# Kernel tuning notes

Hardware: AMD Instinct MI355X
Metric: run time of the kernel (lower is better)

Reference implementation:

```python
import jax, jax.numpy as jnp
import numpy as np

MIN_NORM = 1e-15
EPS = 1e-7  # artanh domain clamp for fp32


def _tan_k(u, k):
    sk = jnp.sqrt(-k)
    return jnp.tanh(jnp.clip(sk * u, -15.0, 15.0)) / sk


def _artan_k(u, k):
    sk = jnp.sqrt(-k)
    return jnp.arctanh(jnp.clip(sk * u, -1.0 + EPS, 1.0 - EPS)) / sk


def _norm(x):
    return jnp.maximum(jnp.linalg.norm(x, axis=-1, keepdims=True), MIN_NORM)


def mobius_add(x, y, k):
    x2 = jnp.sum(x * x, axis=-1, keepdims=True)
    y2 = jnp.sum(y * y, axis=-1, keepdims=True)
    xy = jnp.sum(x * y, axis=-1, keepdims=True)
    num = (1.0 - 2.0 * k * xy - k * y2) * x + (1.0 + k * x2) * y
    den = 1.0 - 2.0 * k * xy + k * k * x2 * y2
    return num / jnp.maximum(den, MIN_NORM)


def mobius_matvec(M, x, k):
    # x: [..., d_in], M: [d_out, d_in]
    xn = _norm(x)
    mx = x @ M.T
    mxn = _norm(mx)
    res = _tan_k(mxn / xn * _artan_k(xn, k), k) * (mx / mxn)
    return jnp.where(jnp.all(mx == 0.0, axis=-1, keepdims=True), 0.0, res)


def mobius_pointwise_mul(w, x, k):
    xn = _norm(x)
    wx = w * x
    wxn = _norm(wx)
    res = _tan_k(wxn / xn * _artan_k(xn, k), k) * (wx / wxn)
    return jnp.where(jnp.all(wx == 0.0, axis=-1, keepdims=True), 0.0, res)


def expmap0(u, k):
    un = _norm(u)
    return _tan_k(un, k) * u / un


def logmap0(y, k):
    yn = _norm(y)
    return _artan_k(yn, k) * y / yn


def one_rnn_transform(W, h, U, x, b, k):
    Wh = mobius_matvec(W, h, k)
    Ux = mobius_matvec(U, x, k)
    return mobius_add(mobius_add(Wh, Ux, k), b, k)


def mobius_gru_cell(x, hx, w_ih, w_hh, b, k):
    W_ir, W_ih_, W_iz = jnp.split(w_ih, 3, axis=0)
    W_hr, W_hh_, W_hz = jnp.split(w_hh, 3, axis=0)
    b_r, b_h, b_z = b[0], b[1], b[2]
    z_t = jax.nn.sigmoid(logmap0(one_rnn_transform(W_hz, hx, W_iz, x, b_z, k), k))
    r_t = jax.nn.sigmoid(logmap0(one_rnn_transform(W_hr, hx, W_ir, x, b_r, k), k))
    rh_t = mobius_pointwise_mul(r_t, hx, k)
    h_tilde = one_rnn_transform(W_hh_, rh_t, W_ih_, x, b_h, k)
    delta_h = mobius_add(-hx, h_tilde, k)
    return mobius_add(hx, mobius_pointwise_mul(z_t, delta_h, k), k)


def mobius_gru_layer(x_tbd, h0, w_ih, w_hh, b, k, hyperbolic_input):
    # x_tbd: [T, B, D]; h0: [B, H]
    if not hyperbolic_input:
        x_tbd = expmap0(x_tbd, k)

    def step(hx, xt):
        h = expmap0(hx, k)
        h = mobius_gru_cell(xt, h, w_ih, w_hh, b, k)
        h = logmap0(h, k)
        return h, h

    h_last, outs = jax.lax.scan(step, h0, x_tbd)
    return outs, h_last  # outs: [T, B, H]


def setup_inputs() -> dict:
    key = jax.random.key(0)
    ks = jax.random.split(key, 8)
    B, T, D, H = 64, 1024, 256, 256
    stdv = 1.0 / np.sqrt(H)
    x = 0.02 * jax.random.normal(ks[0], (B, T, D), dtype=jnp.float32)
    k = jnp.float32(-1.0)  # hyperbolic curvature (geoopt sign convention)
    h0 = jnp.zeros((2, B, H), dtype=jnp.float32)
    w_ih0 = jax.random.uniform(ks[1], (3 * H, D), jnp.float32, -stdv, stdv)
    w_hh0 = jax.random.uniform(ks[2], (3 * H, H), jnp.float32, -stdv, stdv)
    b0 = 1e-5 * jax.random.normal(ks[3], (3, H), dtype=jnp.float32)
    w_ih1 = jax.random.uniform(ks[4], (3 * H, H), jnp.float32, -stdv, stdv)
    w_hh1 = jax.random.uniform(ks[5], (3 * H, H), jnp.float32, -stdv, stdv)
    b1 = 1e-5 * jax.random.normal(ks[6], (3, H), dtype=jnp.float32)
    return {"x": x, "k": k, "h0": h0, "w_ih0": w_ih0, "w_hh0": w_hh0, "b0": b0,
            "w_ih1": w_ih1, "w_hh1": w_hh1, "b1": b1}


def reference(x, k, h0, w_ih0, w_hh0, b0, w_ih1, w_hh1, b1):
    # x: [B, T, D]; source unbinds dim 1 as time -> scan over time-major.
    xt = jnp.swapaxes(x, 0, 1)  # [T, B, D]
    out0, hl0 = mobius_gru_layer(xt, h0[0], w_ih0, w_hh0, b0, k, hyperbolic_input=False)
    out1, hl1 = mobius_gru_layer(out0, h0[1], w_ih1, w_hh1, b1, k, hyperbolic_input=True)
    ht = jnp.stack([hl0, hl1])  # [num_layers, B, H]
    return out1, ht
```

## Files before the change

### kernel.cpp

```cpp
#include <hip/hip_runtime.h>
#include <cstdint>
#include <cstddef>

#define MINN 1e-15f
#define EPSA 1e-7f
#define C_L2E 1.44269504088896341f
#define C_LN2 0.69314718055994531f

typedef _Float16 half_t;
typedef _Float16 half2_t __attribute__((ext_vector_type(2)));

#if defined(__has_builtin)
#if __has_builtin(__builtin_amdgcn_update_dpp) && __has_builtin(__builtin_amdgcn_readlane)
#define USE_DPP 1
#endif
#endif

__device__ __forceinline__ float fexp2_(float x) {
#if defined(__has_builtin) && __has_builtin(__builtin_amdgcn_exp2f)
    return __builtin_amdgcn_exp2f(x);
#else
    return exp2f(x);
#endif
}
__device__ __forceinline__ float flog2_(float x) {
#if defined(__has_builtin) && __has_builtin(__builtin_amdgcn_logf)
    return __builtin_amdgcn_logf(x);
#else
    return log2f(x);
#endif
}
__device__ __forceinline__ float frcp_(float x) {
#if defined(__has_builtin) && __has_builtin(__builtin_amdgcn_rcpf)
    return __builtin_amdgcn_rcpf(x);
#else
    return 1.f / x;
#endif
}
__device__ __forceinline__ float tan_k_(float u, float sk, float rsk) {
    float a = fminf(fmaxf(sk * u, -15.f), 15.f);
    float t = fexp2_(a * (2.f * C_L2E));
    return (1.f - 2.f * frcp_(t + 1.f)) * rsk;
}
__device__ __forceinline__ float artan_k_(float u, float sk, float rsk) {
    float a = fminf(fmaxf(sk * u, -1.f + EPSA), 1.f - EPSA);
    return flog2_((1.f + a) * frcp_(1.f - a)) * (0.5f * C_LN2) * rsk;
}
__device__ __forceinline__ float sigm_(float x) {
    return frcp_(1.f + fexp2_(-x * C_L2E));
}
__device__ __forceinline__ float wave_sum(float v) {
#pragma unroll
    for (int off = 32; off; off >>= 1) v += __shfl_xor(v, off, 64);
    return v;
}

#ifdef USE_DPP
template <int CTRL, int RM, int BM>
__device__ __forceinline__ float dppmov_(float x) {
    return __builtin_bit_cast(float,
        __builtin_amdgcn_update_dpp(0, __builtin_bit_cast(int, x), CTRL, RM, BM, false));
}
#endif
__device__ __forceinline__ float wsum63_(float x) {
#ifdef USE_DPP
    x += dppmov_<0x111, 0xf, 0xf>(x);
    x += dppmov_<0x112, 0xf, 0xf>(x);
    x += dppmov_<0x114, 0xf, 0xe>(x);
    x += dppmov_<0x118, 0xf, 0xc>(x);
    x += dppmov_<0x142, 0xa, 0xf>(x);
    x += dppmov_<0x143, 0xc, 0xf>(x);
    return x;
#else
    return wave_sum(x);
#endif
}
__device__ __forceinline__ float gsum8_(float x) {
#ifdef USE_DPP
    x += dppmov_<0x111, 0xf, 0xf>(x);
    x += dppmov_<0x112, 0xf, 0xf>(x);
    x += dppmov_<0x114, 0xf, 0xe>(x);
    return x;
#else
    x += __shfl_xor(x, 1, 64);
    x += __shfl_xor(x, 2, 64);
    x += __shfl_xor(x, 4, 64);
    return x;
#endif
}
__device__ __forceinline__ float rdlane_(float x, int l) {
#ifdef USE_DPP
    return __builtin_bit_cast(float,
        __builtin_amdgcn_readlane(__builtin_bit_cast(int, x), l));
#else
    return __shfl(x, l, 64);
#endif
}
template <int N>
__device__ __forceinline__ void bredX(float* v, float* redbuf, int tid) {
    const int lane = tid & 63, wave = tid >> 6;
#pragma unroll
    for (int n = 0; n < N; ++n) {
        float s = wsum63_(v[n]);
        if (lane == 63) redbuf[n * 8 + wave] = s;
    }
    __syncthreads();
    float part = redbuf[lane & (8 * N - 1)];
    part = gsum8_(part);
#pragma unroll
    for (int n = 0; n < N; ++n) v[n] = rdlane_(part, 8 * n + 7);
}

__device__ __forceinline__ float dot2acc(uint32_t w, uint32_t h, float acc) {
#if defined(__has_builtin) && __has_builtin(__builtin_amdgcn_fdot2)
    return __builtin_amdgcn_fdot2(__builtin_bit_cast(half2_t, w),
                                  __builtin_bit_cast(half2_t, h), acc, false);
#else
    half2_t a = __builtin_bit_cast(half2_t, w);
    half2_t b = __builtin_bit_cast(half2_t, h);
    acc = fmaf((float)a[0], (float)b[0], acc);
    return fmaf((float)a[1], (float)b[1], acc);
#endif
}

__global__ __launch_bounds__(256) void kt_transpose(
    const float* __restrict__ a0, const float* __restrict__ a1,
    float* __restrict__ o0, float* __restrict__ o1) {
    int idx = blockIdx.x * 256 + threadIdx.x;
    int m = idx / 196608, rem = idx % 196608;
    int j = rem >> 8, kk = rem & 255;
    const float* in = (m == 0) ? a0 : a1;
    float* outp     = (m == 0) ? o0 : o1;
    outp[kk * 768 + j] = in[j * 256 + kk];
}

__global__ __launch_bounds__(256) void kt_prep1(
    const float* __restrict__ whh0, const float* __restrict__ whh1,
    uint32_t* __restrict__ p0, uint32_t* __restrict__ p1) {
    int idx = blockIdx.x * 256 + threadIdx.x;
    int l = idx >> 16, e = idx & 65535;
    int r4 = e >> 11, rem = e & 2047;
    int t = rem >> 2, m = r4 * 4 + (rem & 3);
    int lane = t & 63, wave = t >> 6;
    int p = wave * 32 + (lane & 31), ph = lane >> 5;
    int g = m >> 6, mi = m & 63;
    int row = g ? (512 + p) : p;
    int i = ph * 128 + 2 * mi;
    const float* w = l ? whh1 : whh0;
    half2_t hv;
    hv[0] = (half_t)w[row * 256 + i];
    hv[1] = (half_t)w[row * 256 + i + 1];
    (l ? p1 : p0)[e] = __builtin_bit_cast(uint32_t, hv);
}

__global__ __launch_bounds__(256) void kt_prep2(
    const float* __restrict__ whh0, const float* __restrict__ whh1,
    uint32_t* __restrict__ p0, uint32_t* __restrict__ p1) {
    int idx = blockIdx.x * 256 + threadIdx.x;
    int l = idx >> 15, e = idx & 32767;
    int i2 = e >> 8, j = e & 255;
    const float* w = l ? whh1 : whh0;
    half2_t hv;
    hv[0] = (half_t)w[(256 + j) * 256 + 2 * i2];
    hv[1] = (half_t)w[(256 + j) * 256 + 2 * i2 + 1];
    (l ? p1 : p0)[e] = __builtin_bit_cast(uint32_t, hv);
}

__global__ __launch_bounds__(256) void kt_init(
    const float* __restrict__ h0, float* __restrict__ hcar) {
    int i = blockIdx.x * 256 + threadIdx.x;
    hcar[i] = h0[i];
}
__global__ __launch_bounds__(256) void kt_final(
    const float* __restrict__ hcar, float* __restrict__ dst) {
    int i = blockIdx.x * 256 + threadIdx.x;
    dst[i] = hcar[i];
}

__global__ __launch_bounds__(256) void kt_rowscale(
    const float* __restrict__ src, long long strideB,
    float* __restrict__ s_arr, float* __restrict__ ax_arr,
    const float* __restrict__ kptr, int mode) {
    int lane = threadIdx.x & 63;
    int r = blockIdx.x * 4 + (threadIdx.x >> 6);
    float k = kptr[0], sk = sqrtf(-k), rsk = frcp_(sk);
    size_t off = (size_t)(r >> 6) * strideB + (size_t)(r & 63) * 256 + lane * 4;
    float4 v = *(const float4*)&src[off];
    float n2 = wave_sum(v.x * v.x + v.y * v.y + v.z * v.z + v.w * v.w);
    float n = sqrtf(n2);
    float s, xn;
    if (mode == 0) {
        float nrm = fmaxf(n, MINN);
        float tk = tan_k_(nrm, sk, rsk);
        s = tk * frcp_(nrm);
        xn = fmaxf(tk * (n * frcp_(nrm)), MINN);
    } else {
        s = 1.f;
        xn = fmaxf(n, MINN);
    }
    float ax = artan_k_(xn, sk, rsk) * frcp_(xn);
    if (lane == 0) { s_arr[r] = s; ax_arr[r] = ax; }
}

__global__ __launch_bounds__(256) void kt_gemm(
    const float* __restrict__ A, long long strideB,
    const float* __restrict__ s_arr,
    const float* __restrict__ Bt, float* __restrict__ C) {
    __shared__ float As[16][68];
    __shared__ float Bs[16][68];
    __shared__ float sS[64];
    int tid = threadIdx.x;
    int row0 = blockIdx.y * 64, col0 = blockIdx.x * 64;
    if (tid < 64) sS[tid] = s_arr[row0 + tid];
    int ty = tid >> 4, tx = tid & 15;
    int ra = tid >> 2, kq = tid & 3;
    int kb = tid >> 4, cq = tid & 15;
    float acc[4][4] = {};
    __syncthreads();
#pragma unroll 1
    for (int kt = 0; kt < 16; ++kt) {
        int k0 = kt * 16;
        int rc = row0 + ra;
        size_t aoff = (size_t)(rc >> 6) * strideB + (size_t)(rc & 63) * 256 + k0 + kq * 4;
        float4 av = *(const float4*)&A[aoff];
        float sc = sS[ra];
        float4 bv = *(const float4*)&Bt[(size_t)(k0 + kb) * 768 + col0 + cq * 4];
        As[kq * 4 + 0][ra] = av.x * sc;
        As[kq * 4 + 1][ra] = av.y * sc;
        As[kq * 4 + 2][ra] = av.z * sc;
        As[kq * 4 + 3][ra] = av.w * sc;
        *(float4*)&Bs[kb][cq * 4] = bv;
        __syncthreads();
#pragma unroll
        for (int kk = 0; kk < 16; ++kk) {
            float4 a4 = *(const float4*)&As[kk][ty * 4];
            float4 b4 = *(const float4*)&Bs[kk][tx * 4];
            float aa[4] = {a4.x, a4.y, a4.z, a4.w};
            float bb[4] = {b4.x, b4.y, b4.z, b4.w};
#pragma unroll
            for (int i = 0; i < 4; ++i)
#pragma unroll
                for (int j = 0; j < 4; ++j)
                    acc[i][j] = fmaf(aa[i], bb[j], acc[i][j]);
        }
        __syncthreads();
    }
#pragma unroll
    for (int i = 0; i < 4; ++i) {
        size_t row = (size_t)row0 + ty * 4 + i;
        *(float4*)&C[row * 768 + col0 + tx * 4] =
            make_float4(acc[i][0], acc[i][1], acc[i][2], acc[i][3]);
    }
}

__global__ __launch_bounds__(256) void kt_mscale(
    float* __restrict__ mx, const float* __restrict__ ax_arr,
    float* __restrict__ uxn, float* __restrict__ uxb,
    const float* __restrict__ bias, const float* __restrict__ kptr) {
    int lane = threadIdx.x & 63;
    int p = blockIdx.x * 4 + (threadIdx.x >> 6);
    int r = p / 3;
    int g = p - r * 3;
    float k = kptr[0], sk = sqrtf(-k), rsk = frcp_(sk);
    float* ptr = mx + (size_t)r * 768 + g * 256 + lane * 4;
    float4 v = *(const float4*)ptr;
    float4 b4 = *(const float4*)&bias[g * 256 + lane * 4];
    float n2 = wave_sum(v.x * v.x + v.y * v.y + v.z * v.z + v.w * v.w);
    float vb = wave_sum(v.x * b4.x + v.y * b4.y + v.z * b4.z + v.w * b4.w);
    float nt = sqrtf(n2);
    float mxn = fmaxf(nt, MINN);
    float arg = mxn * ax_arr[r];
    float tk = tan_k_(arg, sk, rsk);
    float f = tk * frcp_(mxn);
    v.x *= f; v.y *= f; v.z *= f; v.w *= f;
    *(float4*)ptr = v;
    if (lane == 0) { uxn[p] = tk * (nt * frcp_(mxn)); uxb[p] = f * vb; }
}

__global__ __launch_bounds__(512, 1) void kt_scan2(
    const float* __restrict__ Ux_0, const float* __restrict__ uxn_0,
    const float* __restrict__ uxb_0,
    const uint32_t* __restrict__ w1pk_0, const uint32_t* __restrict__ whh2g_0,
    const float* __restrict__ bias_0, float* __restrict__ hcar_0,
    float* __restrict__ out_0, long long sb_0, long long st_0,
    const float* __restrict__ Ux_1, const float* __restrict__ uxn_1,
    const float* __restrict__ uxb_1,
    const uint32_t* __restrict__ w1pk_1, const uint32_t* __restrict__ whh2g_1,
    const float* __restrict__ bias_1, float* __restrict__ hcar_1,
    float* __restrict__ out_1, long long sb_1, long long st_1,
    const float* __restrict__ kptr, int Tc, int nrole0) {
    __shared__ uint4 whhS[8192];
    __shared__ uint32_t hy2S[128];
    __shared__ uint32_t rh2S[128];
    __shared__ float redbuf[2][64];

    const int tid = threadIdx.x;
    const int role = (blockIdx.x >= nrole0) ? 1 : 0;
    const int bb = role ? (int)blockIdx.x - nrole0 : (int)blockIdx.x;

    const float* Ux      = role ? Ux_1 : Ux_0;
    const float* uxn     = role ? uxn_1 : uxn_0;
    const float* uxb     = role ? uxb_1 : uxb_0;
    const uint32_t* w1pk = role ? w1pk_1 : w1pk_0;
    const uint32_t* whh2g= role ? whh2g_1 : whh2g_0;
    const float* bias    = role ? bias_1 : bias_0;
    float* hcar          = role ? hcar_1 : hcar_0;
    float* outbase       = role ? out_1 : out_0;
    const long long stride_b = role ? sb_1 : sb_0;
    const long long stride_t = role ? st_1 : st_0;

    const int lane = tid & 63, wave = tid >> 6;
    const int p = wave * 32 + (lane & 31), ph = lane >> 5;
    const float k = kptr[0], sk = sqrtf(-k), rsk = frcp_(sk);

    for (int idx = tid; idx < 32768; idx += 512) {
        uint32_t v = whh2g[idx];
        int i2 = idx >> 8, col = idx & 255;
        ((uint32_t*)whhS)[((i2 >> 2) * 256 + col) * 4 + (i2 & 3)] = v;
    }
    uint32_t w1[128];
    {
        const uint4* wp = (const uint4*)w1pk;
#pragma unroll
        for (int r4 = 0; r4 < 32; ++r4) {
            uint4 v = wp[r4 * 512 + tid];
            w1[4 * r4 + 0] = v.x; w1[4 * r4 + 1] = v.y;
            w1[4 * r4 + 2] = v.z; w1[4 * r4 + 3] = v.w;
        }
    }

    const float br = bias[p], bh = bias[256 + p], bz = bias[512 + p];
    float h = hcar[bb * 256 + p];
    __syncthreads();
    float v4[4] = {br * br, bh * bh, bz * bz, h * h};
    bredX<4>(v4, redbuf[0], tid);
    const float bn2r = 0.5f * v4[0], bn2h = 0.5f * v4[1], bn2z = 0.5f * v4[2];
    float S_h2 = 0.5f * v4[3];

    float* myout = outbase + (size_t)bb * stride_b;
    const float* uxpb = Ux + (size_t)bb * Tc * 768;
    const float* unpb = uxn + (size_t)bb * Tc * 3;
    const float* ubpb = uxb + (size_t)bb * Tc * 3;

    float puxr = uxpb[p], puxh = uxpb[256 + p], puxz = uxpb[512 + p];
    float punr = unpb[0], punh = unpb[1], punz = unpb[2];
    float pubr = ubpb[0], pubh = ubpb[1], pubz = ubpb[2];

    for (int t = 0; t < Tc; ++t) {
        const float uxr = puxr, uxh = puxh, uxz = puxz;
        const float unr = punr, unh = punh, unz = punz;
        const float S_ubr = pubr, S_ubh = pubh, S_ubz = pubz;

        float hn = sqrtf(S_h2);
        float nrm = fmaxf(hn, MINN);
        float tk0 = tan_k_(nrm, sk, rsk);
        float chy = tk0 * frcp_(nrm);
        float hy = chy * h;
        float Shy2 = chy * chy * S_h2;
        float xnh = fmaxf(tk0 * (hn * frcp_(nrm)), MINN);
        float axh = artan_k_(xnh, sk, rsk) * frcp_(xnh);
        if (ph == 0) ((half_t*)hy2S)[p] = (half_t)hy;
        __syncthreads();

        if (t + 1 < Tc) {
            const float* uxp2 = uxpb + (size_t)(t + 1) * 768;
            puxr = uxp2[p]; puxh = uxp2[256 + p]; puxz = uxp2[512 + p];
            const float* unp2 = unpb + (size_t)(t + 1) * 3;
            punr = unp2[0]; punh = unp2[1]; punz = unp2[2];
            const float* ubp2 = ubpb + (size_t)(t + 1) * 3;
            pubr = ubp2[0]; pubh = ubp2[1]; pubz = ubp2[2];
        }

        float pr0 = 0.f, pr1 = 0.f, pz0 = 0.f, pz1 = 0.f;
        {
            const uint4* hp = (const uint4*)hy2S + ph * 16;
#pragma unroll
            for (int c4 = 0; c4 < 4; ++c4) {
                uint32_t hv[16];
#pragma unroll
                for (int u = 0; u < 4; ++u) {
                    uint4 v = hp[c4 * 4 + u];
                    hv[4 * u + 0] = v.x; hv[4 * u + 1] = v.y;
                    hv[4 * u + 2] = v.z; hv[4 * u + 3] = v.w;
                }
#pragma unroll
                for (int m = 0; m < 16; ++m) {
                    if (c4 < 2) {
                        pr0 = dot2acc(w1[c4 * 16 + m], hv[m], pr0);
                        pz0 = dot2acc(w1[64 + c4 * 16 + m], hv[m], pz0);
                    } else {
                        pr1 = dot2acc(w1[c4 * 16 + m], hv[m], pr1);
                        pz1 = dot2acc(w1[64 + c4 * 16 + m], hv[m], pz1);
                    }
                }
            }
        }
        float pr = pr0 + pr1, pz = pz0 + pz1;
        const float mr = pr + __shfl_xor(pr, 32, 64);
        const float mz = pz + __shfl_xor(pz, 32, 64);

        float vr[8] = {mr * mr, mz * mz, mr * uxr, mz * uxz,
                       mr * br, mz * bz, h * uxh, h * bh};
        bredX<8>(vr, redbuf[0], tid);
        const float S_mr2 = 0.5f * vr[0], S_mz2 = 0.5f * vr[1];
        const float S_mru = 0.5f * vr[2], S_mzu = 0.5f * vr[3];
        const float S_mrb = 0.5f * vr[4], S_mzb = 0.5f * vr[5];
        const float S_huxh = 0.5f * vr[6], S_hbh = 0.5f * vr[7];

        float r_t, z_t;
        {
            float mxn = fmaxf(sqrtf(S_mr2), MINN);
            float tk = tan_k_(mxn * axh, sk, rsk);
            float f = tk * frcp_(mxn);
            float x2 = f * f * S_mr2, y2 = unr * unr, xy = f * S_mru;
            float a = 1.f - 2.f * k * xy - k * y2;
            float bq = 1.f + k * x2;
            float rd = frcp_(fmaxf(1.f - 2.f * k * xy + k * k * x2 * y2, MINN));
            float c1 = (a * f * mr + bq * uxr) * rd;
            float Sc12 = (a * a * x2 + 2.f * a * bq * xy + bq * bq * y2) * (rd * rd);
            float Sc1b = (a * f * S_mrb + bq * S_ubr) * rd;
            float g = 1.f - 2.f * k * Sc1b - k * bn2r;
            float dl = 1.f + k * Sc12;
            float re = frcp_(fmaxf(1.f - 2.f * k * Sc1b + k * k * Sc12 * bn2r, MINN));
            float c2 = (g * c1 + dl * br) * re;
            float Sc22 = (g * g * Sc12 + 2.f * g * dl * Sc1b + dl * dl * bn2r) * (re * re);
            float yn = fmaxf(sqrtf(Sc22), MINN);
            float lr = artan_k_(yn, sk, rsk) * frcp_(yn) * c2;
            r_t = sigm_(lr);
        }
        {
            float mxn = fmaxf(sqrtf(S_mz2), MINN);
            float tk = tan_k_(mxn * axh, sk, rsk);
            float f = tk * frcp_(mxn);
            float x2 = f * f * S_mz2, y2 = unz * unz, xy = f * S_mzu;
            float a = 1.f - 2.f * k * xy - k * y2;
            float bq = 1.f + k * x2;
            float rd = frcp_(fmaxf(1.f - 2.f * k * xy + k * k * x2 * y2, MINN));
            float c1 = (a * f * mz + bq * uxz) * rd;
            float Sc12 = (a * a * x2 + 2.f * a * bq * xy + bq * bq * y2) * (rd * rd);
            float Sc1b = (a * f * S_mzb + bq * S_ubz) * rd;
            float g = 1.f - 2.f * k * Sc1b - k * bn2z;
            float dl = 1.f + k * Sc12;
            float re = frcp_(fmaxf(1.f - 2.f * k * Sc1b + k * k * Sc12 * bn2z, MINN));
            float c2 = (g * c1 + dl * bz) * re;
            float Sc22 = (g * g * Sc12 + 2.f * g * dl * Sc1b + dl * dl * bn2z) * (re * re);
            float yn = fmaxf(sqrtf(Sc22), MINN);
            float lz = artan_k_(yn, sk, rsk) * frcp_(yn) * c2;
            z_t = sigm_(lz);
        }

        float wx = r_t * hy;
        if (ph == 0) ((half_t*)rh2S)[p] = (half_t)wx;
        {
            float s1v = wsum63_(wx * wx);
            if (lane == 63) redbuf[1][wave] = s1v;
        }
        __syncthreads();

        float part1 = gsum8_(redbuf[1][lane & 7]);
        const float S_wx2 = 0.5f * rdlane_(part1, 7);
        float wxt = sqrtf(S_wx2);
        float wxn = fmaxf(wxt, MINN);
        float tkw = tan_k_(wxn * axh, sk, rsk);
        float fw = tkw * frcp_(wxn);
        float rhn = tkw * (wxt * frcp_(wxn));

        float q0 = 0.f, q1 = 0.f;
        {
            const uint4* rp = (const uint4*)rh2S + ph * 16;
#pragma unroll
            for (int u = 0; u < 16; ++u) {
                uint4 wv = whhS[(ph * 16 + u) * 256 + p];
                uint4 rv = rp[u];
                if (u < 8) {
                    q0 = dot2acc(wv.x, rv.x, q0);
                    q0 = dot2acc(wv.y, rv.y, q0);
                    q0 = dot2acc(wv.z, rv.z, q0);
                    q0 = dot2acc(wv.w, rv.w, q0);
                } else {
                    q1 = dot2acc(wv.x, rv.x, q1);
                    q1 = dot2acc(wv.y, rv.y, q1);
                    q1 = dot2acc(wv.z, rv.z, q1);
                    q1 = dot2acc(wv.w, rv.w, q1);
                }
            }
        }
        float qq = q0 + q1;
        const float mh = fw * (qq + __shfl_xor(qq, 32, 64));

        float v4b[4] = {mh * mh, mh * uxh, mh * bh, hy * mh};
        bredX<4>(v4b, redbuf[0], tid);
        const float S_mh2 = 0.5f * v4b[0], S_mhu = 0.5f * v4b[1];
        const float S_mhb = 0.5f * v4b[2], S_hymh = 0.5f * v4b[3];

        float wz, Sdelta2;
        {
            float xnrh = fmaxf(rhn, MINN);
            float axrh = artan_k_(xnrh, sk, rsk) * frcp_(xnrh);
            float mxn = fmaxf(sqrtf(S_mh2), MINN);
            float tk = tan_k_(mxn * axrh, sk, rsk);
            float f = tk * frcp_(mxn);
            float x2 = f * f * S_mh2, y2 = unh * unh, xy = f * S_mhu;
            float a = 1.f - 2.f * k * xy - k * y2;
            float bq = 1.f + k * x2;
            float rd = frcp_(fmaxf(1.f - 2.f * k * xy + k * k * x2 * y2, MINN));
            float c1 = (a * f * mh + bq * uxh) * rd;
            float Sc12 = (a * a * x2 + 2.f * a * bq * xy + bq * bq * y2) * (rd * rd);
            float Sc1b = (a * f * S_mhb + bq * S_ubh) * rd;
            float S_hyc1 = (a * f * S_hymh + bq * chy * S_huxh) * rd;
            float g = 1.f - 2.f * k * Sc1b - k * bn2h;
            float dl = 1.f + k * Sc12;
            float re = frcp_(fmaxf(1.f - 2.f * k * Sc1b + k * k * Sc12 * bn2h, MINN));
            float htl = (g * c1 + dl * bh) * re;
            float Shtl2 = (g * g * Sc12 + 2.f * g * dl * Sc1b + dl * dl * bn2h) * (re * re);
            float S_hyhtl = (g * S_hyc1 + dl * chy * S_hbh) * re;
            float ad = 1.f + 2.f * k * S_hyhtl - k * Shtl2;
            float bd = 1.f + k * Shy2;
            float rdd = frcp_(fmaxf(1.f + 2.f * k * S_hyhtl + k * k * Shy2 * Shtl2, MINN));
            float delta = (ad * (-hy) + bd * htl) * rdd;
            Sdelta2 = (ad * ad * Shy2 - 2.f * ad * bd * S_hyhtl + bd * bd * Shtl2) * (rdd * rdd);
            wz = z_t * delta;
        }
        float v2[2] = {wz * wz, hy * wz};
        bredX<2>(v2, redbuf[1], tid);
        const float S_wz2 = 0.5f * v2[0], S_hywz = 0.5f * v2[1];

        {
            float dnc = fmaxf(sqrtf(Sdelta2), MINN);
            float axd = artan_k_(dnc, sk, rsk) * frcp_(dnc);
            float wzt = sqrtf(S_wz2);
            float wznc = fmaxf(wzt, MINN);
            float tkzd = tan_k_(wznc * axd, sk, rsk);
            float fz = tkzd * frcp_(wznc);
            float zd = fz * wz;
            float zdn2 = fz * fz * S_wz2;
            float S_hyzd = fz * S_hywz;
            float an = 1.f - 2.f * k * S_hyzd - k * zdn2;
            float bn_ = 1.f + k * Shy2;
            float rdn = frcp_(fmaxf(1.f - 2.f * k * S_hyzd + k * k * Shy2 * zdn2, MINN));
            float hnew = (an * hy + bn_ * zd) * rdn;
            float Shnew2 = (an * an * Shy2 + 2.f * an * bn_ * S_hyzd + bn_ * bn_ * zdn2) * (rdn * rdn);
            float yn = fmaxf(sqrtf(Shnew2), MINN);
            float ayn = artan_k_(yn, sk, rsk) * frcp_(yn);
            float outv = ayn * hnew;
            if (ph == 0) myout[(size_t)t * stride_t + p] = outv;
            h = outv;
            S_h2 = ayn * ayn * Shnew2;
        }
    }
    if (ph == 0) hcar[bb * 256 + p] = h;
}

extern "C" void kernel_launch(void* const* d_in, const int* in_sizes, int n_in,
                              void* d_out, int out_size, void* d_ws, size_t ws_size,
                              hipStream_t stream) {
    const float* x    = (const float*)d_in[0];
    const float* kptr = (const float*)d_in[1];
    const float* h0   = (const float*)d_in[2];
    const float* wih0 = (const float*)d_in[3];
    const float* whh0 = (const float*)d_in[4];
    const float* b0   = (const float*)d_in[5];
    const float* wih1 = (const float*)d_in[6];
    const float* whh1 = (const float*)d_in[7];
    const float* b1   = (const float*)d_in[8];
    float* out = (float*)d_out;
    float* ws  = (float*)d_ws;

    const int B = 64, T = 1024, H = 256;
    const int CT = 64, NC = 16;
    const int RC = B * CT;

    float* wt_ih0 = ws;
    float* wt_ih1 = wt_ih0 + 196608;
    uint32_t* w1pk0  = (uint32_t*)(wt_ih1 + 196608);
    uint32_t* w1pk1  = w1pk0 + 65536;
    uint32_t* whh2g0 = w1pk1 + 65536;
    uint32_t* whh2g1 = whh2g0 + 32768;
    float* hcar  = (float*)(whh2g1 + 32768);
    float* s0    = hcar + 32768;
    float* ax0   = s0 + RC;
    float* s1    = ax0 + RC;
    float* ax1   = s1 + RC;
    float* uxn0  = ax1 + RC;
    float* uxn1  = uxn0 + 3 * RC;
    float* uxb0  = uxn1 + 3 * RC;
    float* uxb1  = uxb0 + 3 * RC;
    float* out0c = uxb1 + 3 * RC;
    float* mx0   = out0c + (size_t)RC * H;
    float* mx1   = mx0 + (size_t)RC * 768;

    float* hcar0 = hcar;
    float* hcar1 = hcar + (size_t)B * H;

    dim3 blk(256);
    kt_transpose<<<dim3(1536), blk, 0, stream>>>(wih0, wih1, wt_ih0, wt_ih1);
    kt_prep1<<<dim3(512), blk, 0, stream>>>(whh0, whh1, w1pk0, w1pk1);
    kt_prep2<<<dim3(256), blk, 0, stream>>>(whh0, whh1, whh2g0, whh2g1);
    kt_init<<<dim3(128), blk, 0, stream>>>(h0, hcar);

    const long long sbx = (long long)T * 256;
    const long long sbc = (long long)CT * 256;

    {
        const float* xc = x;
        kt_rowscale<<<dim3(RC / 4), blk, 0, stream>>>(xc, sbx, s0, ax0, kptr, 0);
        kt_gemm<<<dim3(12, RC / 64), blk, 0, stream>>>(xc, sbx, s0, wt_ih0, mx0);
        kt_mscale<<<dim3(RC * 3 / 4), blk, 0, stream>>>(mx0, ax0, uxn0, uxb0, b0, kptr);
        kt_scan2<<<dim3(B), dim3(512), 0, stream>>>(
            mx0, uxn0, uxb0, w1pk0, whh2g0, b0, hcar0, out0c, sbc, 256LL,
            mx0, uxn0, uxb0, w1pk0, whh2g0, b0, hcar0, out0c, sbc, 256LL,
            kptr, CT, B);
    }
    for (int c = 1; c < NC; ++c) {
        const float* xc = x + (size_t)c * CT * 256;
        kt_rowscale<<<dim3(RC / 4), blk, 0, stream>>>(xc, sbx, s0, ax0, kptr, 0);
        kt_gemm<<<dim3(12, RC / 64), blk, 0, stream>>>(xc, sbx, s0, wt_ih0, mx0);
        kt_mscale<<<dim3(RC * 3 / 4), blk, 0, stream>>>(mx0, ax0, uxn0, uxb0, b0, kptr);
        kt_rowscale<<<dim3(RC / 4), blk, 0, stream>>>(out0c, sbc, s1, ax1, kptr, 1);
        kt_gemm<<<dim3(12, RC / 64), blk, 0, stream>>>(out0c, sbc, s1, wt_ih1, mx1);
        kt_mscale<<<dim3(RC * 3 / 4), blk, 0, stream>>>(mx1, ax1, uxn1, uxb1, b1, kptr);
        kt_scan2<<<dim3(2 * B), dim3(512), 0, stream>>>(
            mx0, uxn0, uxb0, w1pk0, whh2g0, b0, hcar0, out0c, sbc, 256LL,
            mx1, uxn1, uxb1, w1pk1, whh2g1, b1, hcar1,
            out + (size_t)(c - 1) * CT * B * H, 256LL, (long long)B * H,
            kptr, CT, B);
    }
    {
        kt_rowscale<<<dim3(RC / 4), blk, 0, stream>>>(out0c, sbc, s1, ax1, kptr, 1);
        kt_gemm<<<dim3(12, RC / 64), blk, 0, stream>>>(out0c, sbc, s1, wt_ih1, mx1);
        kt_mscale<<<dim3(RC * 3 / 4), blk, 0, stream>>>(mx1, ax1, uxn1, uxb1, b1, kptr);
        kt_scan2<<<dim3(B), dim3(512), 0, stream>>>(
            mx1, uxn1, uxb1, w1pk1, whh2g1, b1, hcar1,
            out + (size_t)(NC - 1) * CT * B * H, 256LL, (long long)B * H,
            mx1, uxn1, uxb1, w1pk1, whh2g1, b1, hcar1,
            out + (size_t)(NC - 1) * CT * B * H, 256LL, (long long)B * H,
            kptr, CT, B);
    }
    kt_final<<<dim3(128), blk, 0, stream>>>(hcar, out + (size_t)T * B * H);
}
```

Baseline: 6.298 ms.

## Hold all recurrent weights in registers using 1024-thread scan blocks

The recurrent scan kernel now runs with 1024 threads per block, and each thread keeps 96 packed fp16 weight words in registers. Previously each thread held 128 words and the candidate-gate weights were staged in a 128KB shared-memory tile. Each output row is now split across four lane groups instead of two. The block reductions, the weight packing kernel and the gsum helper are widened to 16 waves, and the second prep kernel is removed. This drops the per-step shared-memory weight reads but adds an extra shuffle stage and more waves taking part in each barrier.

```diff
diff --git a/kernel.cpp b/kernel.cpp
--- a/kernel.cpp
+++ b/kernel.cpp
@@ -75,16 +75,18 @@
     return wave_sum(x);
 #endif
 }
-__device__ __forceinline__ float gsum8_(float x) {
+__device__ __forceinline__ float gsum16_(float x) {
 #ifdef USE_DPP
     x += dppmov_<0x111, 0xf, 0xf>(x);
     x += dppmov_<0x112, 0xf, 0xf>(x);
     x += dppmov_<0x114, 0xf, 0xe>(x);
+    x += dppmov_<0x118, 0xf, 0xc>(x);
     return x;
 #else
     x += __shfl_xor(x, 1, 64);
     x += __shfl_xor(x, 2, 64);
     x += __shfl_xor(x, 4, 64);
+    x += __shfl_xor(x, 8, 64);
     return x;
 #endif
 }
@@ -102,13 +104,21 @@
 #pragma unroll
     for (int n = 0; n < N; ++n) {
         float s = wsum63_(v[n]);
-        if (lane == 63) redbuf[n * 8 + wave] = s;
+        if (lane == 63) redbuf[n * 16 + wave] = s;
     }
     __syncthreads();
-    float part = redbuf[lane & (8 * N - 1)];
-    part = gsum8_(part);
-#pragma unroll
-    for (int n = 0; n < N; ++n) v[n] = rdlane_(part, 8 * n + 7);
+    if (N <= 4) {
+        float part = gsum16_(redbuf[lane & (16 * N - 1)]);
+#pragma unroll
+        for (int n = 0; n < N; ++n) v[n] = rdlane_(part, 16 * n + 15);
+    } else {
+        float part0 = gsum16_(redbuf[lane]);
+        float part1 = gsum16_(redbuf[64 + lane]);
+#pragma unroll
+        for (int n = 0; n < N; ++n)
+            v[n] = (n < 4) ? rdlane_(part0, 16 * n + 15)
+                           : rdlane_(part1, 16 * (n - 4) + 15);
+    }
 }
 
 __device__ __forceinline__ float dot2acc(uint32_t w, uint32_t h, float acc) {
@@ -138,31 +148,25 @@
     const float* __restrict__ whh0, const float* __restrict__ whh1,
     uint32_t* __restrict__ p0, uint32_t* __restrict__ p1) {
     int idx = blockIdx.x * 256 + threadIdx.x;
-    int l = idx >> 16, e = idx & 65535;
-    int r4 = e >> 11, rem = e & 2047;
+    int l = idx / 98304, e = idx % 98304;
+    int r4 = e >> 12, rem = e & 4095;
     int t = rem >> 2, m = r4 * 4 + (rem & 3);
     int lane = t & 63, wave = t >> 6;
-    int p = wave * 32 + (lane & 31), ph = lane >> 5;
-    int g = m >> 6, mi = m & 63;
-    int row = g ? (512 + p) : p;
-    int i = ph * 128 + 2 * mi;
+    int p = wave * 16 + (lane & 15), ph = lane >> 4;
+    int row, i;
+    if (m < 64) {
+        int g = m >> 5, mi = m & 31;
+        row = g ? (512 + p) : p;
+        i = 64 * ph + 2 * mi;
+    } else {
+        int mi = m - 64;
+        row = 256 + p;
+        i = 64 * ph + 2 * mi;
+    }
     const float* w = l ? whh1 : whh0;
     half2_t hv;
     hv[0] = (half_t)w[row * 256 + i];
     hv[1] = (half_t)w[row * 256 + i + 1];
-    (l ? p1 : p0)[e] = __builtin_bit_cast(uint32_t, hv);
-}
-
-__global__ __launch_bounds__(256) void kt_prep2(
-    const float* __restrict__ whh0, const float* __restrict__ whh1,
-    uint32_t* __restrict__ p0, uint32_t* __restrict__ p1) {
-    int idx = blockIdx.x * 256 + threadIdx.x;
-    int l = idx >> 15, e = idx & 32767;
-    int i2 = e >> 8, j = e & 255;
-    const float* w = l ? whh1 : whh0;
-    half2_t hv;
-    hv[0] = (half_t)w[(256 + j) * 256 + 2 * i2];
-    hv[1] = (half_t)w[(256 + j) * 256 + 2 * i2 + 1];
     (l ? p1 : p0)[e] = __builtin_bit_cast(uint32_t, hv);
 }
 
@@ -277,22 +281,19 @@
     if (lane == 0) { uxn[p] = tk * (nt * frcp_(mxn)); uxb[p] = f * vb; }
 }
 
-__global__ __launch_bounds__(512, 1) void kt_scan2(
+__global__ __launch_bounds__(1024, 1) void kt_scan2(
     const float* __restrict__ Ux_0, const float* __restrict__ uxn_0,
-    const float* __restrict__ uxb_0,
-    const uint32_t* __restrict__ w1pk_0, const uint32_t* __restrict__ whh2g_0,
+    const float* __restrict__ uxb_0, const uint32_t* __restrict__ w1pk_0,
     const float* __restrict__ bias_0, float* __restrict__ hcar_0,
     float* __restrict__ out_0, long long sb_0, long long st_0,
     const float* __restrict__ Ux_1, const float* __restrict__ uxn_1,
-    const float* __restrict__ uxb_1,
-    const uint32_t* __restrict__ w1pk_1, const uint32_t* __restrict__ whh2g_1,
+    const float* __restrict__ uxb_1, const uint32_t* __restrict__ w1pk_1,
     const float* __restrict__ bias_1, float* __restrict__ hcar_1,
     float* __restrict__ out_1, long long sb_1, long long st_1,
     const float* __restrict__ kptr, int Tc, int nrole0) {
-    __shared__ uint4 whhS[8192];
     __shared__ uint32_t hy2S[128];
     __shared__ uint32_t rh2S[128];
-    __shared__ float redbuf[2][64];
+    __shared__ float redbuf[2][128];
 
     const int tid = threadIdx.x;
     const int role = (blockIdx.x >= nrole0) ? 1 : 0;
@@ -302,7 +303,6 @@
     const float* uxn     = role ? uxn_1 : uxn_0;
     const float* uxb     = role ? uxb_1 : uxb_0;
     const uint32_t* w1pk = role ? w1pk_1 : w1pk_0;
-    const uint32_t* whh2g= role ? whh2g_1 : whh2g_0;
     const float* bias    = role ? bias_1 : bias_0;
     float* hcar          = role ? hcar_1 : hcar_0;
     float* outbase       = role ? out_1 : out_0;
@@ -310,20 +310,16 @@
     const long long stride_t = role ? st_1 : st_0;
 
     const int lane = tid & 63, wave = tid >> 6;
-    const int p = wave * 32 + (lane & 31), ph = lane >> 5;
+    const int p = wave * 16 + (lane & 15);
+    const int ph = lane >> 4;
     const float k = kptr[0], sk = sqrtf(-k), rsk = frcp_(sk);
 
-    for (int idx = tid; idx < 32768; idx += 512) {
-        uint32_t v = whh2g[idx];
-        int i2 = idx >> 8, col = idx & 255;
-        ((uint32_t*)whhS)[((i2 >> 2) * 256 + col) * 4 + (i2 & 3)] = v;
-    }
-    uint32_t w1[128];
+    uint32_t w1[96];
     {
         const uint4* wp = (const uint4*)w1pk;
 #pragma unroll
-        for (int r4 = 0; r4 < 32; ++r4) {
-            uint4 v = wp[r4 * 512 + tid];
+        for (int r4 = 0; r4 < 24; ++r4) {
+            uint4 v = wp[r4 * 1024 + tid];
             w1[4 * r4 + 0] = v.x; w1[4 * r4 + 1] = v.y;
             w1[4 * r4 + 2] = v.z; w1[4 * r4 + 3] = v.w;
         }
@@ -334,8 +330,8 @@
     __syncthreads();
     float v4[4] = {br * br, bh * bh, bz * bz, h * h};
     bredX<4>(v4, redbuf[0], tid);
-    const float bn2r = 0.5f * v4[0], bn2h = 0.5f * v4[1], bn2z = 0.5f * v4[2];
-    float S_h2 = 0.5f * v4[3];
+    const float bn2r = 0.25f * v4[0], bn2h = 0.25f * v4[1], bn2z = 0.25f * v4[2];
+    float S_h2 = 0.25f * v4[3];
 
     float* myout = outbase + (size_t)bb * stride_b;
     const float* uxpb = Ux + (size_t)bb * Tc * 768;
@@ -359,7 +355,7 @@
         float Shy2 = chy * chy * S_h2;
         float xnh = fmaxf(tk0 * (hn * frcp_(nrm)), MINN);
         float axh = artan_k_(xnh, sk, rsk) * frcp_(xnh);
-        if (ph == 0) ((half_t*)hy2S)[p] = (half_t)hy;
+        if (lane < 16) ((half_t*)hy2S)[p] = (half_t)hy;
         __syncthreads();
 
         if (t + 1 < Tc) {
@@ -373,39 +369,46 @@
 
         float pr0 = 0.f, pr1 = 0.f, pz0 = 0.f, pz1 = 0.f;
         {
-            const uint4* hp = (const uint4*)hy2S + ph * 16;
-#pragma unroll
-            for (int c4 = 0; c4 < 4; ++c4) {
-                uint32_t hv[16];
-#pragma unroll
-                for (int u = 0; u < 4; ++u) {
-                    uint4 v = hp[c4 * 4 + u];
-                    hv[4 * u + 0] = v.x; hv[4 * u + 1] = v.y;
-                    hv[4 * u + 2] = v.z; hv[4 * u + 3] = v.w;
-                }
-#pragma unroll
-                for (int m = 0; m < 16; ++m) {
-                    if (c4 < 2) {
-                        pr0 = dot2acc(w1[c4 * 16 + m], hv[m], pr0);
-                        pz0 = dot2acc(w1[64 + c4 * 16 + m], hv[m], pz0);
-                    } else {
-                        pr1 = dot2acc(w1[c4 * 16 + m], hv[m], pr1);
-                        pz1 = dot2acc(w1[64 + c4 * 16 + m], hv[m], pz1);
-                    }
+            const uint4* hp = (const uint4*)hy2S + 8 * ph;
+            uint4 hvv[8];
+#pragma unroll
+            for (int u = 0; u < 8; ++u) hvv[u] = hp[u];
+#pragma unroll
+            for (int u = 0; u < 8; ++u) {
+                uint32_t a0 = hvv[u].x, a1 = hvv[u].y, a2 = hvv[u].z, a3 = hvv[u].w;
+                if (u & 1) {
+                    pr1 = dot2acc(w1[4 * u + 0], a0, pr1);
+                    pr1 = dot2acc(w1[4 * u + 1], a1, pr1);
+                    pr1 = dot2acc(w1[4 * u + 2], a2, pr1);
+                    pr1 = dot2acc(w1[4 * u + 3], a3, pr1);
+                    pz1 = dot2acc(w1[32 + 4 * u + 0], a0, pz1);
+                    pz1 = dot2acc(w1[32 + 4 * u + 1], a1, pz1);
+                    pz1 = dot2acc(w1[32 + 4 * u + 2], a2, pz1);
+                    pz1 = dot2acc(w1[32 + 4 * u + 3], a3, pz1);
+                } else {
+                    pr0 = dot2acc(w1[4 * u + 0], a0, pr0);
+                    pr0 = dot2acc(w1[4 * u + 1], a1, pr0);
+                    pr0 = dot2acc(w1[4 * u + 2], a2, pr0);
+                    pr0 = dot2acc(w1[4 * u + 3], a3, pr0);
+                    pz0 = dot2acc(w1[32 + 4 * u + 0], a0, pz0);
+                    pz0 = dot2acc(w1[32 + 4 * u + 1], a1, pz0);
+                    pz0 = dot2acc(w1[32 + 4 * u + 2], a2, pz0);
+                    pz0 = dot2acc(w1[32 + 4 * u + 3], a3, pz0);
                 }
             }
         }
         float pr = pr0 + pr1, pz = pz0 + pz1;
-        const float mr = pr + __shfl_xor(pr, 32, 64);
-        const float mz = pz + __shfl_xor(pz, 32, 64);
+        pr += __shfl_xor(pr, 16, 64); pr += __shfl_xor(pr, 32, 64);
+        pz += __shfl_xor(pz, 16, 64); pz += __shfl_xor(pz, 32, 64);
+        const float mr = pr, mz = pz;
 
         float vr[8] = {mr * mr, mz * mz, mr * uxr, mz * uxz,
                        mr * br, mz * bz, h * uxh, h * bh};
         bredX<8>(vr, redbuf[0], tid);
-        const float S_mr2 = 0.5f * vr[0], S_mz2 = 0.5f * vr[1];
-        const float S_mru = 0.5f * vr[2], S_mzu = 0.5f * vr[3];
-        const float S_mrb = 0.5f * vr[4], S_mzb = 0.5f * vr[5];
-        const float S_huxh = 0.5f * vr[6], S_hbh = 0.5f * vr[7];
+        const float S_mr2 = 0.25f * vr[0], S_mz2 = 0.25f * vr[1];
+        const float S_mru = 0.25f * vr[2], S_mzu = 0.25f * vr[3];
+        const float S_mrb = 0.25f * vr[4], S_mzb = 0.25f * vr[5];
+        const float S_huxh = 0.25f * vr[6], S_hbh = 0.25f * vr[7];
 
         float r_t, z_t;
         {
@@ -450,15 +453,15 @@
         }
 
         float wx = r_t * hy;
-        if (ph == 0) ((half_t*)rh2S)[p] = (half_t)wx;
+        if (lane < 16) ((half_t*)rh2S)[p] = (half_t)wx;
         {
             float s1v = wsum63_(wx * wx);
             if (lane == 63) redbuf[1][wave] = s1v;
         }
         __syncthreads();
 
-        float part1 = gsum8_(redbuf[1][lane & 7]);
-        const float S_wx2 = 0.5f * rdlane_(part1, 7);
+        float part1 = gsum16_(redbuf[1][lane & 15]);
+        const float S_wx2 = 0.25f * rdlane_(part1, 15);
         float wxt = sqrtf(S_wx2);
         float wxn = fmaxf(wxt, MINN);
         float tkw = tan_k_(wxn * axh, sk, rsk);
@@ -467,31 +470,34 @@
 
         float q0 = 0.f, q1 = 0.f;
         {
-            const uint4* rp = (const uint4*)rh2S + ph * 16;
-#pragma unroll
-            for (int u = 0; u < 16; ++u) {
-                uint4 wv = whhS[(ph * 16 + u) * 256 + p];
-                uint4 rv = rp[u];
-                if (u < 8) {
-                    q0 = dot2acc(wv.x, rv.x, q0);
-                    q0 = dot2acc(wv.y, rv.y, q0);
-                    q0 = dot2acc(wv.z, rv.z, q0);
-                    q0 = dot2acc(wv.w, rv.w, q0);
+            const uint4* rp = (const uint4*)rh2S + 8 * ph;
+            uint4 rvv[8];
+#pragma unroll
+            for (int u = 0; u < 8; ++u) rvv[u] = rp[u];
+#pragma unroll
+            for (int u = 0; u < 8; ++u) {
+                uint32_t a0 = rvv[u].x, a1 = rvv[u].y, a2 = rvv[u].z, a3 = rvv[u].w;
+                if (u & 1) {
+                    q1 = dot2acc(w1[64 + 4 * u + 0], a0, q1);
+                    q1 = dot2acc(w1[64 + 4 * u + 1], a1, q1);
+                    q1 = dot2acc(w1[64 + 4 * u + 2], a2, q1);
+                    q1 = dot2acc(w1[64 + 4 * u + 3], a3, q1);
                 } else {
-                    q1 = dot2acc(wv.x, rv.x, q1);
-                    q1 = dot2acc(wv.y, rv.y, q1);
-                    q1 = dot2acc(wv.z, rv.z, q1);
-                    q1 = dot2acc(wv.w, rv.w, q1);
+                    q0 = dot2acc(w1[64 + 4 * u + 0], a0, q0);
+                    q0 = dot2acc(w1[64 + 4 * u + 1], a1, q0);
+                    q0 = dot2acc(w1[64 + 4 * u + 2], a2, q0);
+                    q0 = dot2acc(w1[64 + 4 * u + 3], a3, q0);
                 }
             }
         }
         float qq = q0 + q1;
-        const float mh = fw * (qq + __shfl_xor(qq, 32, 64));
+        qq += __shfl_xor(qq, 16, 64); qq += __shfl_xor(qq, 32, 64);
+        const float mh = fw * qq;
 
         float v4b[4] = {mh * mh, mh * uxh, mh * bh, hy * mh};
         bredX<4>(v4b, redbuf[0], tid);
-        const float S_mh2 = 0.5f * v4b[0], S_mhu = 0.5f * v4b[1];
-        const float S_mhb = 0.5f * v4b[2], S_hymh = 0.5f * v4b[3];
+        const float S_mh2 = 0.25f * v4b[0], S_mhu = 0.25f * v4b[1];
+        const float S_mhb = 0.25f * v4b[2], S_hymh = 0.25f * v4b[3];
 
         float wz, Sdelta2;
         {
@@ -523,7 +529,7 @@
         }
         float v2[2] = {wz * wz, hy * wz};
         bredX<2>(v2, redbuf[1], tid);
-        const float S_wz2 = 0.5f * v2[0], S_hywz = 0.5f * v2[1];
+        const float S_wz2 = 0.25f * v2[0], S_hywz = 0.25f * v2[1];
 
         {
             float dnc = fmaxf(sqrtf(Sdelta2), MINN);
@@ -543,12 +549,12 @@
             float yn = fmaxf(sqrtf(Shnew2), MINN);
             float ayn = artan_k_(yn, sk, rsk) * frcp_(yn);
             float outv = ayn * hnew;
-            if (ph == 0) myout[(size_t)t * stride_t + p] = outv;
+            if (lane < 16) myout[(size_t)t * stride_t + p] = outv;
             h = outv;
             S_h2 = ayn * ayn * Shnew2;
         }
     }
-    if (ph == 0) hcar[bb * 256 + p] = h;
+    if (lane < 16) hcar[bb * 256 + p] = h;
 }
 
 extern "C" void kernel_launch(void* const* d_in, const int* in_sizes, int n_in,
@@ -572,11 +578,9 @@
 
     float* wt_ih0 = ws;
     float* wt_ih1 = wt_ih0 + 196608;
-    uint32_t* w1pk0  = (uint32_t*)(wt_ih1 + 196608);
-    uint32_t* w1pk1  = w1pk0 + 65536;
-    uint32_t* whh2g0 = w1pk1 + 65536;
-    uint32_t* whh2g1 = whh2g0 + 32768;
-    float* hcar  = (float*)(whh2g1 + 32768);
+    uint32_t* w1pk0 = (uint32_t*)(wt_ih1 + 196608);
+    uint32_t* w1pk1 = w1pk0 + 98304;
+    float* hcar  = (float*)(w1pk1 + 98304);
     float* s0    = hcar + 32768;
     float* ax0   = s0 + RC;
     float* s1    = ax0 + RC;
@@ -594,8 +598,7 @@
 
     dim3 blk(256);
     kt_transpose<<<dim3(1536), blk, 0, stream>>>(wih0, wih1, wt_ih0, wt_ih1);
-    kt_prep1<<<dim3(512), blk, 0, stream>>>(whh0, whh1, w1pk0, w1pk1);
-    kt_prep2<<<dim3(256), blk, 0, stream>>>(whh0, whh1, whh2g0, whh2g1);
+    kt_prep1<<<dim3(768), blk, 0, stream>>>(whh0, whh1, w1pk0, w1pk1);
     kt_init<<<dim3(128), blk, 0, stream>>>(h0, hcar);
 
     const long long sbx = (long long)T * 256;
@@ -606,9 +609,9 @@
         kt_rowscale<<<dim3(RC / 4), blk, 0, stream>>>(xc, sbx, s0, ax0, kptr, 0);
         kt_gemm<<<dim3(12, RC / 64), blk, 0, stream>>>(xc, sbx, s0, wt_ih0, mx0);
         kt_mscale<<<dim3(RC * 3 / 4), blk, 0, stream>>>(mx0, ax0, uxn0, uxb0, b0, kptr);
-        kt_scan2<<<dim3(B), dim3(512), 0, stream>>>(
-            mx0, uxn0, uxb0, w1pk0, whh2g0, b0, hcar0, out0c, sbc, 256LL,
-            mx0, uxn0, uxb0, w1pk0, whh2g0, b0, hcar0, out0c, sbc, 256LL,
+        kt_scan2<<<dim3(B), dim3(1024), 0, stream>>>(
+            mx0, uxn0, uxb0, w1pk0, b0, hcar0, out0c, sbc, 256LL,
+            mx0, uxn0, uxb0, w1pk0, b0, hcar0, out0c, sbc, 256LL,
             kptr, CT, B);
     }
     for (int c = 1; c < NC; ++c) {
@@ -619,9 +622,9 @@
         kt_rowscale<<<dim3(RC / 4), blk, 0, stream>>>(out0c, sbc, s1, ax1, kptr, 1);
         kt_gemm<<<dim3(12, RC / 64), blk, 0, stream>>>(out0c, sbc, s1, wt_ih1, mx1);
         kt_mscale<<<dim3(RC * 3 / 4), blk, 0, stream>>>(mx1, ax1, uxn1, uxb1, b1, kptr);
-        kt_scan2<<<dim3(2 * B), dim3(512), 0, stream>>>(
-            mx0, uxn0, uxb0, w1pk0, whh2g0, b0, hcar0, out0c, sbc, 256LL,
-            mx1, uxn1, uxb1, w1pk1, whh2g1, b1, hcar1,
+        kt_scan2<<<dim3(2 * B), dim3(1024), 0, stream>>>(
+            mx0, uxn0, uxb0, w1pk0, b0, hcar0, out0c, sbc, 256LL,
+            mx1, uxn1, uxb1, w1pk1, b1, hcar1,
             out + (size_t)(c - 1) * CT * B * H, 256LL, (long long)B * H,
             kptr, CT, B);
     }
@@ -629,10 +632,10 @@
         kt_rowscale<<<dim3(RC / 4), blk, 0, stream>>>(out0c, sbc, s1, ax1, kptr, 1);
         kt_gemm<<<dim3(12, RC / 64), blk, 0, stream>>>(out0c, sbc, s1, wt_ih1, mx1);
         kt_mscale<<<dim3(RC * 3 / 4), blk, 0, stream>>>(mx1, ax1, uxn1, uxb1, b1, kptr);
-        kt_scan2<<<dim3(B), dim3(512), 0, stream>>>(
-            mx1, uxn1, uxb1, w1pk1, whh2g1, b1, hcar1,
+        kt_scan2<<<dim3(B), dim3(1024), 0, stream>>>(
+            mx1, uxn1, uxb1, w1pk1, b1, hcar1,
             out + (size_t)(NC - 1) * CT * B * H, 256LL, (long long)B * H,
-            mx1, uxn1, uxb1, w1pk1, whh2g1, b1, hcar1,
+            mx1, uxn1, uxb1, w1pk1, b1, hcar1,
             out + (size_t)(NC - 1) * CT * B * H, 256LL, (long long)B * H,
             kptr, CT, B);
     }
```

New measurement: 13.33 ms. +111.7%, slower.
